# Performance work log

Hardware: AMD Instinct MI355X
Metric: run time of the kernel (lower is better)

## Reference

```python
import jax, jax.numpy as jnp
import numpy as np

K = 15                # top-k codes per token
COMMITMENT_COST = 0.25
N, D, Q = 16384, 256, 8192  # tokens, embed_dim, quant_dim (codebook size)


def setup_inputs() -> dict:
    key = jax.random.key(0)
    k1, k2 = jax.random.split(key)
    z_e = jax.random.normal(k1, (N, D), dtype=jnp.float32)
    # codebook initialized uniform(-1/Q, 1/Q) as in the torch module
    embedding = jax.random.uniform(k2, (Q, D), dtype=jnp.float32,
                                   minval=-1.0 / Q, maxval=1.0 / Q)
    return {"z_e": z_e, "embedding": embedding}


def reference(z_e, embedding):
    # squared L2 distances: [N, Q]
    dist = (jnp.sum(z_e ** 2, axis=1, keepdims=True)
            - 2.0 * (z_e @ embedding.T)
            + jnp.sum(embedding ** 2, axis=1)[None, :])
    # top-k nearest codes (torch.topk(-dist))
    _, top_k_indices = jax.lax.top_k(-dist, K)           # [N, K] int32
    z_q_k = embedding[top_k_indices]                      # [N, K, D] gather
    # k-hot scatter: [N, Q]
    rows = jnp.arange(z_e.shape[0])[:, None]              # [N, 1]
    k_hot = jnp.zeros((z_e.shape[0], embedding.shape[0]), dtype=z_e.dtype)
    k_hot = k_hot.at[rows, top_k_indices].set(1.0)
    z_q = jnp.sum(z_q_k, axis=1)                          # [N, D]
    vq_loss = jnp.mean((z_q - jax.lax.stop_gradient(z_e)) ** 2)
    commitment_loss = jnp.mean((z_e - jax.lax.stop_gradient(z_q)) ** 2)
    total_vq_loss = vq_loss + COMMITMENT_COST * commitment_loss
    # straight-through estimator
    z_q_ste = z_e + jax.lax.stop_gradient(z_q - z_e)
    return (z_q_ste, total_vq_loss, k_hot)
```

## Files before the change

### kernel.cpp

```cpp
#include <hip/hip_runtime.h>


#pragma clang fp contract(off)

#define DIM   256
#define KSEL  15
#define CAP   160
#define NTC   32
#define NTO   32
#define KR    24

typedef short  s16x8 __attribute__((ext_vector_type(8)));
typedef float  f32x4 __attribute__((ext_vector_type(4)));

__device__ inline unsigned short f2bf(float f) {
  unsigned u = __builtin_bit_cast(unsigned, f);
  unsigned r = (u + 0x7FFFu + ((u >> 16) & 1u)) >> 16;
  return (unsigned short)r;
}

__device__ inline void nt_zero4(float* p) {
  f32x4 v = {0.f, 0.f, 0.f, 0.f};
  __builtin_nontemporal_store(v, (f32x4*)p);
}

__global__ __launch_bounds__(256)
void prep(const float* __restrict__ emb, unsigned short* __restrict__ ebf,
          float* __restrict__ Enp, int Q) {
  const int gid = blockIdx.x * 256 + threadIdx.x;
  {
    const int i = gid * 8;
    float4 a = *(const float4*)(emb + i);
    float4 b = *(const float4*)(emb + i + 4);
    ushort4 o0; o0.x = f2bf(a.x); o0.y = f2bf(a.y); o0.z = f2bf(a.z); o0.w = f2bf(a.w);
    ushort4 o1; o1.x = f2bf(b.x); o1.y = f2bf(b.y); o1.z = f2bf(b.z); o1.w = f2bf(b.w);
    *(ushort4*)(ebf + i) = o0;
    *(ushort4*)(ebf + i + 4) = o1;
  }
  if (gid < Q) {
    const float* ep = emb + (size_t)gid * DIM;
    float Eh[2];
    for (int h = 0; h < 2; ++h) {
      const int base = 128 * h;
      float r[8];
#pragma unroll
      for (int q2 = 0; q2 < 8; ++q2) { float v = ep[base + q2]; r[q2] = v * v; }
      for (int i = 8; i < 128; i += 8)
#pragma unroll
        for (int q2 = 0; q2 < 8; ++q2) { float v = ep[base + i + q2]; float sq = v * v; r[q2] = r[q2] + sq; }
      Eh[h] = ((r[0] + r[1]) + (r[2] + r[3])) + ((r[4] + r[5]) + (r[6] + r[7]));
    }
    Enp[gid] = Eh[0] + Eh[1];
  }
}

__global__ __launch_bounds__(256, 3)
void vq_capture(const float* __restrict__ z, const unsigned short* __restrict__ ebf,
                int* __restrict__ cntg, unsigned short* __restrict__ candg,
                float* __restrict__ out, int N, int Q) {
  __shared__ unsigned short zbf[NTC][264];
  __shared__ unsigned short candL[NTC][CAP + 2];
  __shared__ float scL[NTC][CAP + 1];
  __shared__ int   cntL[NTC];
  __shared__ float tauL[NTC];
  __shared__ float red[256];

  const int tid  = threadIdx.x;
  const int lane = tid & 63;
  const int wv   = tid >> 6;
  const int t0   = blockIdx.x * NTC;
  float* khot = out + (size_t)N * DIM + 1;

  {
    const int rt = tid >> 3, rq = tid & 7;
    const float* zp = z + (size_t)(t0 + rt) * DIM;
    float s = 0.f;
#pragma unroll
    for (int m = 0; m < 8; ++m) {
      float4 v = *(const float4*)(zp + 4 * rq + 32 * m);
      s = __builtin_fmaf(v.x, v.x, s);
      s = __builtin_fmaf(v.y, v.y, s);
      s = __builtin_fmaf(v.z, v.z, s);
      s = __builtin_fmaf(v.w, v.w, s);
      ushort4 o; o.x = f2bf(v.x); o.y = f2bf(v.y); o.z = f2bf(v.z); o.w = f2bf(v.w);
      *(ushort4*)&zbf[rt][4 * rq + 32 * m] = o;
    }
    red[tid] = s;
  }
  if (tid < NTC) cntL[tid] = 0;
  if (tid < 3) khot[(size_t)t0 * Q + tid] = 0.f;
  if (tid == 3) khot[(size_t)t0 * Q + (size_t)NTC * Q - 1] = 0.f;
  __syncthreads();

  if (tid < NTC) {
    float s = 0.f;
    for (int j = 0; j < 8; ++j) s += red[tid * 8 + j];
    const float a = 1.0f / (float)Q;
    tauL[tid] = 2.45f * a * 0.57735027f * sqrtf(s) - 1e-6f;
  }
  __syncthreads();

  s16x8 afrag[2][8];
  {
    const int arow = lane & 15;
    const int kq   = (lane >> 4) * 8;
#pragma unroll
    for (int tt = 0; tt < 2; ++tt) {
#pragma unroll
      for (int ks = 0; ks < 8; ++ks)
        afrag[tt][ks] = *(const s16x8*)&zbf[tt * 16 + arow][ks * 32 + kq];
    }
  }

  {
    const int ncw  = Q / 4;
    const int c0w  = wv * ncw;
    const int col  = lane & 15;
    const int kq8  = (lane >> 4) * 8;
    const int rbase = (lane >> 4) * 4;
    const unsigned short* bbase = ebf + ((size_t)(c0w + col) * DIM + kq8);
    float* pref = khot + (size_t)t0 * Q + 3;
    const int nf4 = (NTC * Q - 4) / 4;

    uint4 buf0[8], buf1[8];
#pragma unroll
    for (int ks = 0; ks < 8; ++ks) buf0[ks] = *(const uint4*)(bbase + ks * 32);

    for (int it = 0; it < 128; it += 2) {
      {
        const unsigned short* bp = bbase + (size_t)(it + 1) * 16 * DIM;
#pragma unroll
        for (int ks = 0; ks < 8; ++ks) buf1[ks] = *(const uint4*)(bp + ks * 32);
      }
      {
        const int i0 = it * 512 + tid, i1 = i0 + 256;
        if (i0 < nf4) nt_zero4(pref + 4 * i0);
        if (i1 < nf4) nt_zero4(pref + 4 * i1);
      }
      {
        f32x4 acc0 = {0.f, 0.f, 0.f, 0.f};
        f32x4 acc1 = {0.f, 0.f, 0.f, 0.f};
#pragma unroll
        for (int ks = 0; ks < 8; ++ks) {
          s16x8 bfv = __builtin_bit_cast(s16x8, buf0[ks]);
          acc0 = __builtin_amdgcn_mfma_f32_16x16x32_bf16(afrag[0][ks], bfv, acc0, 0, 0, 0);
          acc1 = __builtin_amdgcn_mfma_f32_16x16x32_bf16(afrag[1][ks], bfv, acc1, 0, 0, 0);
        }
        const int code = c0w + it * 16 + col;
#pragma unroll
        for (int r = 0; r < 4; ++r) {
          const int tk0 = rbase + r;
          if (acc0[r] > tauL[tk0]) {
            int s = atomicAdd(&cntL[tk0], 1);
            if (s < CAP) { candL[tk0][s] = (unsigned short)code; scL[tk0][s] = acc0[r]; }
          }
          const int tk1 = 16 + rbase + r;
          if (acc1[r] > tauL[tk1]) {
            int s = atomicAdd(&cntL[tk1], 1);
            if (s < CAP) { candL[tk1][s] = (unsigned short)code; scL[tk1][s] = acc1[r]; }
          }
        }
      }
      if (it + 2 < 128) {
        const unsigned short* bp = bbase + (size_t)(it + 2) * 16 * DIM;
#pragma unroll
        for (int ks = 0; ks < 8; ++ks) buf0[ks] = *(const uint4*)(bp + ks * 32);
      }
      {
        const int i0 = (it + 1) * 512 + tid, i1 = i0 + 256;
        if (i0 < nf4) nt_zero4(pref + 4 * i0);
        if (i1 < nf4) nt_zero4(pref + 4 * i1);
      }
      {
        f32x4 acc0 = {0.f, 0.f, 0.f, 0.f};
        f32x4 acc1 = {0.f, 0.f, 0.f, 0.f};
#pragma unroll
        for (int ks = 0; ks < 8; ++ks) {
          s16x8 bfv = __builtin_bit_cast(s16x8, buf1[ks]);
          acc0 = __builtin_amdgcn_mfma_f32_16x16x32_bf16(afrag[0][ks], bfv, acc0, 0, 0, 0);
          acc1 = __builtin_amdgcn_mfma_f32_16x16x32_bf16(afrag[1][ks], bfv, acc1, 0, 0, 0);
        }
        const int code = c0w + (it + 1) * 16 + col;
#pragma unroll
        for (int r = 0; r < 4; ++r) {
          const int tk0 = rbase + r;
          if (acc0[r] > tauL[tk0]) {
            int s = atomicAdd(&cntL[tk0], 1);
            if (s < CAP) { candL[tk0][s] = (unsigned short)code; scL[tk0][s] = acc0[r]; }
          }
          const int tk1 = 16 + rbase + r;
          if (acc1[r] > tauL[tk1]) {
            int s = atomicAdd(&cntL[tk1], 1);
            if (s < CAP) { candL[tk1][s] = (unsigned short)code; scL[tk1][s] = acc1[r]; }
          }
        }
      }
    }
  }
  __syncthreads();

  if (tid < NTC) {
    const int m = min(cntL[tid], CAP);
    const int keep = min(m, KR);
    for (int k = 0; k < keep; ++k) {
      float bv = -3.4e38f; int bj = 0;
      for (int j = 0; j < m; ++j) {
        float v = scL[tid][j];
        if (v > bv) { bv = v; bj = j; }
      }
      scL[tid][bj] = -3.5e38f;
      candg[(size_t)(t0 + tid) * KR + k] = candL[tid][bj];
    }
    cntg[t0 + tid] = keep;
  }
}

__global__ __launch_bounds__(256, 2)
void vq_out(const float* __restrict__ z, const float* __restrict__ emb,
            const float* __restrict__ Enp, const int* __restrict__ cntg,
            const unsigned short* __restrict__ candg, float* __restrict__ out,
            int N, int Q) {
  __shared__ __align__(16) float zlds[NTO][DIM + 4];
  __shared__ __align__(16) float ebuf[KR][DIM + 4];
  __shared__ unsigned short cand[NTO][KR];
  __shared__ float sc[NTO][KR + 1];
  __shared__ int   cntL[NTO];
  __shared__ float ArowL[NTO];
  __shared__ int   win[NTO][KSEL];
  __shared__ float red[256];

  const int tid = threadIdx.x;
  const int t0  = blockIdx.x * NTO;
  float* khot = out + (size_t)N * DIM + 1;

  {
    const int rt = tid >> 3, rq = tid & 7;
    const float* zp = z + (size_t)(t0 + rt) * DIM;
    float4 tmp[8];
#pragma unroll
    for (int m = 0; m < 8; ++m) tmp[m] = *(const float4*)(zp + 4 * rq + 32 * m);
#pragma unroll
    for (int m = 0; m < 8; ++m) *(float4*)&zlds[rt][4 * rq + 32 * m] = tmp[m];
  }
  if (tid < NTO) cntL[tid] = min(cntg[t0 + tid], KR);
  __syncthreads();

  for (int i = tid; i < NTO * KR; i += 256) {
    const int t = i / KR, s = i - t * KR;
    cand[t][s] = candg[(size_t)(t0 + t) * KR + s];
  }

  if (tid < NTO) {
    const float* zl = &zlds[tid][0];
    float Ah[2];
    for (int h = 0; h < 2; ++h) {
      const int base = 128 * h;
      float r[8];
#pragma unroll
      for (int q2 = 0; q2 < 8; ++q2) { float v = zl[base + q2]; r[q2] = v * v; }
      for (int i = 8; i < 128; i += 8)
#pragma unroll
        for (int q2 = 0; q2 < 8; ++q2) { float v = zl[base + i + q2]; float sq = v * v; r[q2] = r[q2] + sq; }
      Ah[h] = ((r[0] + r[1]) + (r[2] + r[3])) + ((r[4] + r[5]) + (r[6] + r[7]));
    }
    ArowL[tid] = Ah[0] + Ah[1];
  }
  __syncthreads();

  for (int b = 0; b < NTO; ++b) {
    const int mb = cntL[b];
    {
      const int row = tid >> 3, rq = tid & 7;
      if (row < mb) {
        const float* ep = emb + (size_t)cand[b][row] * DIM;
        float4 tmp[8];
#pragma unroll
        for (int m = 0; m < 8; ++m) tmp[m] = *(const float4*)(ep + 4 * rq + 32 * m);
#pragma unroll
        for (int m = 0; m < 8; ++m) *(float4*)&ebuf[row][4 * rq + 32 * m] = tmp[m];
      }
    }
    __syncthreads();
    if ((tid & 7) == 0) {
      const int ci = tid >> 3;
      if (ci < mb) {
        const float* el = &ebuf[ci][0];
        const float* zl = &zlds[b][0];
        float bch = 0.f;
        for (int i = 0; i < 256; i += 8) {
          float4 ea = *(const float4*)(el + i);
          float4 eb = *(const float4*)(el + i + 4);
          float4 za = *(const float4*)(zl + i);
          float4 zb = *(const float4*)(zl + i + 4);
          bch = __builtin_fmaf(za.x, ea.x, bch);
          bch = __builtin_fmaf(za.y, ea.y, bch);
          bch = __builtin_fmaf(za.z, ea.z, bch);
          bch = __builtin_fmaf(za.w, ea.w, bch);
          bch = __builtin_fmaf(zb.x, eb.x, bch);
          bch = __builtin_fmaf(zb.y, eb.y, bch);
          bch = __builtin_fmaf(zb.z, eb.z, bch);
          bch = __builtin_fmaf(zb.w, eb.w, bch);
        }
        const int c = cand[b][ci];
        sc[b][ci] = (ArowL[b] - 2.0f * bch) + Enp[c];
      } else if (ci < KR) {
        sc[b][ci] = 3.4e38f;
      }
    }
    __syncthreads();
  }

  if (tid < NTO) {
    const int m = cntL[tid];
    for (int k = 0; k < KSEL; ++k) {
      float bv = 3.4e38f; int bc = 0x7fffffff; int bj = -1;
      for (int j = 0; j < m; ++j) {
        float v = sc[tid][j]; int c = cand[tid][j];
        if (v < bv || (v == bv && c < bc)) { bv = v; bc = c; bj = j; }
      }
      if (bj >= 0) sc[tid][bj] = 3.5e38f;
      win[tid][k] = (bj >= 0) ? bc : 0;
    }
  }
  __syncthreads();

  {
    const int qt = tid >> 3, qq = tid & 7;
    float4 zq4[8];
#pragma unroll
    for (int m = 0; m < 8; ++m) zq4[m] = make_float4(0.f, 0.f, 0.f, 0.f);
    for (int k = 0; k < KSEL; ++k) {
      const int c = win[qt][k];
      const float* ep = emb + (size_t)c * DIM;
#pragma unroll
      for (int m = 0; m < 8; ++m) {
        float4 e4 = *(const float4*)(ep + 4 * qq + 32 * m);
        zq4[m].x = zq4[m].x + e4.x; zq4[m].y = zq4[m].y + e4.y;
        zq4[m].z = zq4[m].z + e4.z; zq4[m].w = zq4[m].w + e4.w;
      }
    }
    float* op = out + (size_t)(t0 + qt) * DIM;
    float lp = 0.f;
#pragma unroll
    for (int m = 0; m < 8; ++m) {
      float4 zv = *(const float4*)&zlds[qt][4 * qq + 32 * m];
      float4 qv = zq4[m];
      float d0 = qv.x - zv.x, d1 = qv.y - zv.y, d2 = qv.z - zv.z, d3 = qv.w - zv.w;
      float4 o; o.x = zv.x + d0; o.y = zv.y + d1; o.z = zv.z + d2; o.w = zv.w + d3;
      *(float4*)(op + 4 * qq + 32 * m) = o;
      lp = __builtin_fmaf(d0, d0, lp);
      lp = __builtin_fmaf(d1, d1, lp);
      lp = __builtin_fmaf(d2, d2, lp);
      lp = __builtin_fmaf(d3, d3, lp);
    }
    red[tid] = lp;
  }
  __syncthreads();
  for (int s = 128; s > 0; s >>= 1) {
    if (tid < s) red[tid] += red[tid + s];
    __syncthreads();
  }
  if (tid == 0) {
    const float scale = 1.25f / (float)((size_t)N * DIM);
    atomicAdd(out + (size_t)N * DIM, red[0] * scale);
  }

  for (int i = tid; i < NTO * KSEL; i += 256) {
    const int t = i / KSEL, k = i - t * KSEL;
    khot[(size_t)(t0 + t) * Q + win[t][k]] = 1.0f;
  }
}

extern "C" void kernel_launch(void* const* d_in, const int* in_sizes, int n_in,
                              void* d_out, int out_size, void* d_ws, size_t ws_size,
                              hipStream_t stream) {
  const float* z   = (const float*)d_in[0];
  const float* emb = (const float*)d_in[1];
  float* out = (float*)d_out;
  const int N = in_sizes[0] / DIM;
  const int Q = in_sizes[1] / DIM;

  unsigned short* ebf = (unsigned short*)d_ws;
  char* p = (char*)d_ws + (size_t)Q * DIM * 2;
  float* Enp  = (float*)p;           p += (size_t)Q * 4;
  int*   cntg = (int*)p;             p += (size_t)N * 4;
  unsigned short* candg = (unsigned short*)p;

  hipMemsetAsync((char*)d_out + (size_t)N * DIM * sizeof(float), 0, sizeof(float), stream);
  prep<<<dim3((Q * DIM) / (8 * 256)), dim3(256), 0, stream>>>(emb, ebf, Enp, Q);
  vq_capture<<<dim3(N / NTC), dim3(256), 0, stream>>>(z, ebf, cntg, candg, out, N, Q);
  vq_out<<<dim3(N / NTO), dim3(256), 0, stream>>>(z, emb, Enp, cntg, candg, out, N, Q);
}
```

Baseline: 914.8 us.

## Double token tile in capture kernel and move k-hot zeroing into output kernel

The capture kernel now handles 64 tokens per block with 512 threads, so each wave computes four 16-token MFMA tiles per codebook B-fragment load and each wave covers half as many codes. This halves codebook reads per token. The bf16 z staging buffer is unioned with the candidate buffers to hold LDS size down. The non-temporal zeroing of the large k-hot output moves from the capture loop into the vq_out kernel, taking store traffic out of the MFMA loop, at the cost of more register pressure (four A tiles) and a heavier output kernel.

```diff
diff --git a/kernel.cpp b/kernel.cpp
--- a/kernel.cpp
+++ b/kernel.cpp
@@ -6,7 +6,7 @@
 #define DIM   256
 #define KSEL  15
 #define CAP   160
-#define NTC   32
+#define NTC   64
 #define NTO   32
 #define KR    24
 
@@ -54,22 +54,25 @@
   }
 }
 
-__global__ __launch_bounds__(256, 3)
+__global__ __launch_bounds__(512, 2)
 void vq_capture(const float* __restrict__ z, const unsigned short* __restrict__ ebf,
                 int* __restrict__ cntg, unsigned short* __restrict__ candg,
-                float* __restrict__ out, int N, int Q) {
-  __shared__ unsigned short zbf[NTC][264];
-  __shared__ unsigned short candL[NTC][CAP + 2];
-  __shared__ float scL[NTC][CAP + 1];
+                int N, int Q) {
+  __shared__ union {
+    unsigned short zbf[NTC][264];
+    struct {
+      unsigned short candL[NTC][CAP + 2];
+      float          scL[NTC][CAP + 1];
+    } c;
+  } U;
   __shared__ int   cntL[NTC];
   __shared__ float tauL[NTC];
-  __shared__ float red[256];
+  __shared__ float red[512];
 
   const int tid  = threadIdx.x;
   const int lane = tid & 63;
   const int wv   = tid >> 6;
   const int t0   = blockIdx.x * NTC;
-  float* khot = out + (size_t)N * DIM + 1;
 
   {
     const int rt = tid >> 3, rq = tid & 7;
@@ -83,13 +86,11 @@
       s = __builtin_fmaf(v.z, v.z, s);
       s = __builtin_fmaf(v.w, v.w, s);
       ushort4 o; o.x = f2bf(v.x); o.y = f2bf(v.y); o.z = f2bf(v.z); o.w = f2bf(v.w);
-      *(ushort4*)&zbf[rt][4 * rq + 32 * m] = o;
+      *(ushort4*)&U.zbf[rt][4 * rq + 32 * m] = o;
     }
     red[tid] = s;
   }
   if (tid < NTC) cntL[tid] = 0;
-  if (tid < 3) khot[(size_t)t0 * Q + tid] = 0.f;
-  if (tid == 3) khot[(size_t)t0 * Q + (size_t)NTC * Q - 1] = 0.f;
   __syncthreads();
 
   if (tid < NTC) {
@@ -98,53 +99,50 @@
     const float a = 1.0f / (float)Q;
     tauL[tid] = 2.45f * a * 0.57735027f * sqrtf(s) - 1e-6f;
   }
-  __syncthreads();
-
-  s16x8 afrag[2][8];
+
+  s16x8 afrag[4][8];
   {
     const int arow = lane & 15;
     const int kq   = (lane >> 4) * 8;
 #pragma unroll
-    for (int tt = 0; tt < 2; ++tt) {
+    for (int tt = 0; tt < 4; ++tt) {
 #pragma unroll
       for (int ks = 0; ks < 8; ++ks)
-        afrag[tt][ks] = *(const s16x8*)&zbf[tt * 16 + arow][ks * 32 + kq];
-    }
-  }
-
-  {
-    const int ncw  = Q / 4;
+        afrag[tt][ks] = *(const s16x8*)&U.zbf[tt * 16 + arow][ks * 32 + kq];
+    }
+  }
+  __syncthreads();
+
+  {
+    const int ncw  = Q / 8;
     const int c0w  = wv * ncw;
     const int col  = lane & 15;
     const int kq8  = (lane >> 4) * 8;
     const int rbase = (lane >> 4) * 4;
     const unsigned short* bbase = ebf + ((size_t)(c0w + col) * DIM + kq8);
-    float* pref = khot + (size_t)t0 * Q + 3;
-    const int nf4 = (NTC * Q - 4) / 4;
 
     uint4 buf0[8], buf1[8];
 #pragma unroll
     for (int ks = 0; ks < 8; ++ks) buf0[ks] = *(const uint4*)(bbase + ks * 32);
 
-    for (int it = 0; it < 128; it += 2) {
+    for (int it = 0; it < 64; it += 2) {
       {
         const unsigned short* bp = bbase + (size_t)(it + 1) * 16 * DIM;
 #pragma unroll
         for (int ks = 0; ks < 8; ++ks) buf1[ks] = *(const uint4*)(bp + ks * 32);
-      }
-      {
-        const int i0 = it * 512 + tid, i1 = i0 + 256;
-        if (i0 < nf4) nt_zero4(pref + 4 * i0);
-        if (i1 < nf4) nt_zero4(pref + 4 * i1);
       }
       {
         f32x4 acc0 = {0.f, 0.f, 0.f, 0.f};
         f32x4 acc1 = {0.f, 0.f, 0.f, 0.f};
+        f32x4 acc2 = {0.f, 0.f, 0.f, 0.f};
+        f32x4 acc3 = {0.f, 0.f, 0.f, 0.f};
 #pragma unroll
         for (int ks = 0; ks < 8; ++ks) {
           s16x8 bfv = __builtin_bit_cast(s16x8, buf0[ks]);
           acc0 = __builtin_amdgcn_mfma_f32_16x16x32_bf16(afrag[0][ks], bfv, acc0, 0, 0, 0);
           acc1 = __builtin_amdgcn_mfma_f32_16x16x32_bf16(afrag[1][ks], bfv, acc1, 0, 0, 0);
+          acc2 = __builtin_amdgcn_mfma_f32_16x16x32_bf16(afrag[2][ks], bfv, acc2, 0, 0, 0);
+          acc3 = __builtin_amdgcn_mfma_f32_16x16x32_bf16(afrag[3][ks], bfv, acc3, 0, 0, 0);
         }
         const int code = c0w + it * 16 + col;
 #pragma unroll
@@ -152,33 +150,42 @@
           const int tk0 = rbase + r;
           if (acc0[r] > tauL[tk0]) {
             int s = atomicAdd(&cntL[tk0], 1);
-            if (s < CAP) { candL[tk0][s] = (unsigned short)code; scL[tk0][s] = acc0[r]; }
+            if (s < CAP) { U.c.candL[tk0][s] = (unsigned short)code; U.c.scL[tk0][s] = acc0[r]; }
           }
           const int tk1 = 16 + rbase + r;
           if (acc1[r] > tauL[tk1]) {
             int s = atomicAdd(&cntL[tk1], 1);
-            if (s < CAP) { candL[tk1][s] = (unsigned short)code; scL[tk1][s] = acc1[r]; }
+            if (s < CAP) { U.c.candL[tk1][s] = (unsigned short)code; U.c.scL[tk1][s] = acc1[r]; }
+          }
+          const int tk2 = 32 + rbase + r;
+          if (acc2[r] > tauL[tk2]) {
+            int s = atomicAdd(&cntL[tk2], 1);
+            if (s < CAP) { U.c.candL[tk2][s] = (unsigned short)code; U.c.scL[tk2][s] = acc2[r]; }
+          }
+          const int tk3 = 48 + rbase + r;
+          if (acc3[r] > tauL[tk3]) {
+            int s = atomicAdd(&cntL[tk3], 1);
+            if (s < CAP) { U.c.candL[tk3][s] = (unsigned short)code; U.c.scL[tk3][s] = acc3[r]; }
           }
         }
       }
-      if (it + 2 < 128) {
+      if (it + 2 < 64) {
         const unsigned short* bp = bbase + (size_t)(it + 2) * 16 * DIM;
 #pragma unroll
         for (int ks = 0; ks < 8; ++ks) buf0[ks] = *(const uint4*)(bp + ks * 32);
-      }
-      {
-        const int i0 = (it + 1) * 512 + tid, i1 = i0 + 256;
-        if (i0 < nf4) nt_zero4(pref + 4 * i0);
-        if (i1 < nf4) nt_zero4(pref + 4 * i1);
       }
       {
         f32x4 acc0 = {0.f, 0.f, 0.f, 0.f};
         f32x4 acc1 = {0.f, 0.f, 0.f, 0.f};
+        f32x4 acc2 = {0.f, 0.f, 0.f, 0.f};
+        f32x4 acc3 = {0.f, 0.f, 0.f, 0.f};
 #pragma unroll
         for (int ks = 0; ks < 8; ++ks) {
           s16x8 bfv = __builtin_bit_cast(s16x8, buf1[ks]);
           acc0 = __builtin_amdgcn_mfma_f32_16x16x32_bf16(afrag[0][ks], bfv, acc0, 0, 0, 0);
           acc1 = __builtin_amdgcn_mfma_f32_16x16x32_bf16(afrag[1][ks], bfv, acc1, 0, 0, 0);
+          acc2 = __builtin_amdgcn_mfma_f32_16x16x32_bf16(afrag[2][ks], bfv, acc2, 0, 0, 0);
+          acc3 = __builtin_amdgcn_mfma_f32_16x16x32_bf16(afrag[3][ks], bfv, acc3, 0, 0, 0);
         }
         const int code = c0w + (it + 1) * 16 + col;
 #pragma unroll
@@ -186,12 +193,22 @@
           const int tk0 = rbase + r;
           if (acc0[r] > tauL[tk0]) {
             int s = atomicAdd(&cntL[tk0], 1);
-            if (s < CAP) { candL[tk0][s] = (unsigned short)code; scL[tk0][s] = acc0[r]; }
+            if (s < CAP) { U.c.candL[tk0][s] = (unsigned short)code; U.c.scL[tk0][s] = acc0[r]; }
           }
           const int tk1 = 16 + rbase + r;
           if (acc1[r] > tauL[tk1]) {
             int s = atomicAdd(&cntL[tk1], 1);
-            if (s < CAP) { candL[tk1][s] = (unsigned short)code; scL[tk1][s] = acc1[r]; }
+            if (s < CAP) { U.c.candL[tk1][s] = (unsigned short)code; U.c.scL[tk1][s] = acc1[r]; }
+          }
+          const int tk2 = 32 + rbase + r;
+          if (acc2[r] > tauL[tk2]) {
+            int s = atomicAdd(&cntL[tk2], 1);
+            if (s < CAP) { U.c.candL[tk2][s] = (unsigned short)code; U.c.scL[tk2][s] = acc2[r]; }
+          }
+          const int tk3 = 48 + rbase + r;
+          if (acc3[r] > tauL[tk3]) {
+            int s = atomicAdd(&cntL[tk3], 1);
+            if (s < CAP) { U.c.candL[tk3][s] = (unsigned short)code; U.c.scL[tk3][s] = acc3[r]; }
           }
         }
       }
@@ -199,19 +216,20 @@
   }
   __syncthreads();
 
-  if (tid < NTC) {
-    const int m = min(cntL[tid], CAP);
+  if ((tid & 7) == 0) {
+    const int t = tid >> 3;
+    const int m = min(cntL[t], CAP);
     const int keep = min(m, KR);
     for (int k = 0; k < keep; ++k) {
       float bv = -3.4e38f; int bj = 0;
       for (int j = 0; j < m; ++j) {
-        float v = scL[tid][j];
+        float v = U.c.scL[t][j];
         if (v > bv) { bv = v; bj = j; }
       }
-      scL[tid][bj] = -3.5e38f;
-      candg[(size_t)(t0 + tid) * KR + k] = candL[tid][bj];
-    }
-    cntg[t0 + tid] = keep;
+      U.c.scL[t][bj] = -3.5e38f;
+      candg[(size_t)(t0 + t) * KR + k] = U.c.candL[t][bj];
+    }
+    cntg[t0 + t] = keep;
   }
 }
 
@@ -232,6 +250,11 @@
   const int tid = threadIdx.x;
   const int t0  = blockIdx.x * NTO;
   float* khot = out + (size_t)N * DIM + 1;
+  float* pref = khot + (size_t)t0 * Q + 3;
+  const int nf4 = (NTO * Q - 4) / 4;
+
+  if (tid < 3) khot[(size_t)t0 * Q + tid] = 0.f;
+  if (tid == 3) khot[(size_t)t0 * Q + (size_t)NTO * Q - 1] = 0.f;
 
   {
     const int rt = tid >> 3, rq = tid & 7;
@@ -278,6 +301,14 @@
         for (int m = 0; m < 8; ++m) tmp[m] = *(const float4*)(ep + 4 * rq + 32 * m);
 #pragma unroll
         for (int m = 0; m < 8; ++m) *(float4*)&ebuf[row][4 * rq + 32 * m] = tmp[m];
+      }
+    }
+    {
+      const int i0 = b * 2048 + tid;
+#pragma unroll
+      for (int k = 0; k < 8; ++k) {
+        const int i = i0 + k * 256;
+        if (i < nf4) nt_zero4(pref + 4 * (size_t)i);
       }
     }
     __syncthreads();
@@ -388,6 +419,6 @@
 
   hipMemsetAsync((char*)d_out + (size_t)N * DIM * sizeof(float), 0, sizeof(float), stream);
   prep<<<dim3((Q * DIM) / (8 * 256)), dim3(256), 0, stream>>>(emb, ebf, Enp, Q);
-  vq_capture<<<dim3(N / NTC), dim3(256), 0, stream>>>(z, ebf, cntg, candg, out, N, Q);
+  vq_capture<<<dim3(N / NTC), dim3(512), 0, stream>>>(z, ebf, cntg, candg, N, Q);
   vq_out<<<dim3(N / NTO), dim3(256), 0, stream>>>(z, emb, Enp, cntg, candg, out, N, Q);
 }
```

Result: faster. 896.0 us (-2.1%).
